# Optimization experiments

Measured on AMD Instinct MI355X. Metric: run time of the kernel, lower is better.

## Reference

```python
import jax, jax.numpy as jnp
import numpy as np

N_USERS, N_BOOKS, D, E, B = 50000, 100000, 128, 500000, 16384
N = N_USERS + N_BOOKS
EPS = 1e-5


def _gcn_conv(x, W, b, src, dst, n):
    # PyG GCNConv: linear transform, then symmetric-normalized aggregation with self-loops.
    h = x @ W  # [N, D]
    ones = jnp.ones(src.shape[0], h.dtype)
    deg = jax.ops.segment_sum(ones, dst, num_segments=n) + 1.0  # +1 for self-loop
    dis = jax.lax.rsqrt(deg)  # deg^{-1/2}
    norm = dis[src] * dis[dst]  # [E]
    agg = jax.ops.segment_sum(h[src] * norm[:, None], dst, num_segments=n)
    agg = agg + h * (dis * dis)[:, None]  # self-loop contribution, norm = deg_i^{-1}
    return agg + b


def _batch_norm(x, gamma, beta):
    m = x.mean(axis=0)
    v = x.var(axis=0)  # biased, as in torch BN normalization
    return (x - m) * jax.lax.rsqrt(v + EPS) * gamma + beta


def setup_inputs() -> dict:
    key = jax.random.key(0)
    ks = jax.random.split(key, 12)
    edge_index = jax.random.randint(ks[0], (2, E), 0, N)
    x = jax.random.normal(ks[1], (1, 1), dtype=jnp.float32)  # unused by forward
    src_nodes = jax.random.randint(ks[2], (B,), 0, N_USERS)
    dst_nodes = jax.random.randint(ks[3], (B,), N_USERS, N)
    user_emb = 0.01 * jax.random.normal(ks[4], (N_USERS, D), dtype=jnp.float32)
    book_emb = 0.01 * jax.random.normal(ks[5], (N_BOOKS, D), dtype=jnp.float32)
    s = 1.0 / np.sqrt(D)
    W1 = jax.random.uniform(ks[6], (D, D), jnp.float32, -s, s)
    b1 = jnp.zeros((D,), jnp.float32)
    W2 = jax.random.uniform(ks[7], (D, D), jnp.float32, -s, s)
    b2 = jnp.zeros((D,), jnp.float32)
    g1 = jnp.ones((D,), jnp.float32)
    be1 = jnp.zeros((D,), jnp.float32)
    g2 = jnp.ones((D,), jnp.float32)
    be2 = jnp.zeros((D,), jnp.float32)
    return {"edge_index": edge_index, "x": x, "src_nodes": src_nodes,
            "dst_nodes": dst_nodes, "user_emb": user_emb, "book_emb": book_emb,
            "W1": W1, "b1": b1, "g1": g1, "be1": be1,
            "W2": W2, "b2": b2, "g2": g2, "be2": be2}


def reference(edge_index, x, src_nodes, dst_nodes, user_emb, book_emb,
              W1, b1, g1, be1, W2, b2, g2, be2):
    esrc, edst = edge_index[0], edge_index[1]
    h = jnp.concatenate([user_emb, book_emb], axis=0)  # [N, D]
    h = _gcn_conv(h, W1, b1, esrc, edst, N)
    h = jax.nn.relu(_batch_norm(h, g1, be1))
    h = _gcn_conv(h, W2, b2, esrc, edst, N)
    h = jax.nn.relu(_batch_norm(h, g2, be2))
    ratings = jnp.sum(h[src_nodes] * h[dst_nodes], axis=1)  # [B]
    return ratings
```

## Files before the change

### kernel.cpp

```cpp
#include <hip/hip_runtime.h>
#include <hip/hip_bf16.h>

#define NN      150000
#define NUSERS  50000
#define DD      128
#define EE      500000
#define BB      16384
#define NSLICE  32
#define ESTRIDE 32

using short8  = __attribute__((ext_vector_type(8))) short;
using ushort8 = __attribute__((ext_vector_type(8))) unsigned short;
using f32x4   = __attribute__((ext_vector_type(4))) float;

typedef __attribute__((address_space(1))) const unsigned int glb_u32;
typedef __attribute__((address_space(3))) unsigned int       lds_u32;

__device__ __forceinline__ short f2bf(float v) {
    __hip_bfloat16 b = __float2bfloat16(v);
    return __builtin_bit_cast(short, b);
}
__device__ __forceinline__ float bf2f(unsigned short b) {
    return __uint_as_float(((unsigned)b) << 16);
}

__global__ __launch_bounds__(256) void prep_k(int4* __restrict__ zbase, int zn4, int zb,
                                              const float* __restrict__ W1,
                                              const float* __restrict__ W2,
                                              short* __restrict__ F1,
                                              short* __restrict__ F2) {
    int b = blockIdx.x;
    if (b < zb) {
        int i = b * 256 + threadIdx.x;
        if (i < zn4) zbase[i] = make_int4(0, 0, 0, 0);
        return;
    }
    int idx = (b - zb) * 256 + threadIdx.x;
    int m = idx >> 14;
    int i = idx & 16383;
    int e  = i & 7;
    int l  = (i >> 3) & 63;
    int kk = (i >> 9) & 3;
    int ct = i >> 11;
    int k = kk * 32 + (l >> 4) * 8 + e;
    int c = ct * 16 + (l & 15);
    const float* W = m ? W2 : W1;
    short*       F = m ? F2 : F1;
    F[i] = f2bf(W[k * DD + c]);
}

__global__ __launch_bounds__(256) void countfill_k(const int* __restrict__ src,
                                                   const int* __restrict__ dst,
                                                   int* __restrict__ cnt,
                                                   int* __restrict__ sedge,
                                                   const int* __restrict__ srcn,
                                                   const int* __restrict__ dstn,
                                                   unsigned char* __restrict__ flags) {
    int e = blockIdx.x * 256 + threadIdx.x;
    if (e < EE) {
        int d = dst[e], s = src[e];
        int pos = atomicAdd(&cnt[d], 1);
        if (pos > ESTRIDE - 1) pos = ESTRIDE - 1;
        sedge[(size_t)d * ESTRIDE + pos] = s;
    }
    if (e < BB) { flags[srcn[e]] = 1; flags[dstn[e]] = 1; }
}

__global__ __launch_bounds__(256) void dis_k(const int* __restrict__ cnt,
                                             float* __restrict__ dis) {
    int i = blockIdx.x * 256 + threadIdx.x;
    if (i < NN) dis[i] = rsqrtf((float)cnt[i] + 1.0f);
}

template<int MODE>
__global__ __launch_bounds__(128) void gemm_mfma_k(const float* __restrict__ A0,
                                                   const float* __restrict__ A1,
                                                   int nsplit,
                                                   const unsigned short* __restrict__ Ab,
                                                   const float* __restrict__ coefs,
                                                   const short* __restrict__ Wfrag,
                                                   unsigned short* __restrict__ hout) {
    constexpr int ROWB  = (MODE == 0) ? 528 : 272;
    constexpr int PAY   = (MODE == 0) ? 512 : 256;
    constexpr int TILEB = 32 * ROWB;
    constexpr int NCH   = TILEB / 16;
    constexpr int FULLR = NCH / 128;

    __shared__ __align__(16) char smem[TILEB];

    int t    = threadIdx.x;
    int wave = t >> 6;
    int lane = t & 63;
    int kgrp = lane >> 4;
    int lrow = lane & 15;
    int r0   = blockIdx.x * 32;

#pragma unroll
    for (int r = 0; r < FULLR; ++r) {
        int chunk = r * 128 + t;
        int o     = chunk * 16;
        int row   = o / ROWB;
        int inner = o - row * ROWB;
        if (inner >= PAY) inner = 0;
        int gr = r0 + row; if (gr > NN - 1) gr = NN - 1;
        const char* src;
        if (MODE == 0) src = (const char*)((gr < nsplit) ? (A0 + (size_t)gr * DD)
                                                         : (A1 + (size_t)(gr - nsplit) * DD)) + inner;
        else           src = (const char*)(Ab + (size_t)gr * DD) + inner;
        lds_u32* dst = (lds_u32*)(smem + (r * 128 + wave * 64) * 16);
        __builtin_amdgcn_global_load_lds((glb_u32*)src, dst, 16, 0, 0);
    }
    if (wave == 0 && lane < 32) {
        int chunk = FULLR * 128 + lane;
        int o     = chunk * 16;
        int row   = o / ROWB;
        int inner = o - row * ROWB;
        if (inner >= PAY) inner = 0;
        int gr = r0 + row; if (gr > NN - 1) gr = NN - 1;
        const char* src;
        if (MODE == 0) src = (const char*)((gr < nsplit) ? (A0 + (size_t)gr * DD)
                                                         : (A1 + (size_t)(gr - nsplit) * DD)) + inner;
        else           src = (const char*)(Ab + (size_t)gr * DD) + inner;
        lds_u32* dst = (lds_u32*)(smem + FULLR * 128 * 16);
        __builtin_amdgcn_global_load_lds((glb_u32*)src, dst, 16, 0, 0);
    }
    __syncthreads();

    const char* arow = smem + (wave * 16 + lrow) * ROWB;

    f32x4 acc[8];
#pragma unroll
    for (int ct = 0; ct < 8; ++ct) acc[ct] = (f32x4){0.f, 0.f, 0.f, 0.f};

    const short8* wf = (const short8*)Wfrag;

#pragma unroll
    for (int kk = 0; kk < 4; ++kk) {
        short8 rfrag;
        if (MODE == 0) {
            f32x4 va = *(const f32x4*)(arow + kk * 128 + kgrp * 32);
            f32x4 vb = *(const f32x4*)(arow + kk * 128 + kgrp * 32 + 16);
#pragma unroll
            for (int j = 0; j < 4; ++j) { rfrag[j] = f2bf(va[j]); rfrag[4 + j] = f2bf(vb[j]); }
        } else {
            int d0 = kk * 32 + kgrp * 8;
            ushort8 u = *(const ushort8*)(arow + kk * 64 + kgrp * 16);
            f32x4 s1 = *(const f32x4*)(coefs + d0);
            f32x4 s2 = *(const f32x4*)(coefs + d0 + 4);
            f32x4 t1 = *(const f32x4*)(coefs + 128 + d0);
            f32x4 t2 = *(const f32x4*)(coefs + 128 + d0 + 4);
#pragma unroll
            for (int j = 0; j < 4; ++j) {
                rfrag[j]     = f2bf(fmaxf(bf2f(u[j])     * s1[j] + t1[j], 0.f));
                rfrag[4 + j] = f2bf(fmaxf(bf2f(u[4 + j]) * s2[j] + t2[j], 0.f));
            }
        }
#pragma unroll
        for (int ct = 0; ct < 8; ++ct) {
            short8 wfr = wf[(ct * 4 + kk) * 64 + lane];
            acc[ct] = __builtin_amdgcn_mfma_f32_16x16x32_bf16(wfr, rfrag, acc[ct], 0, 0, 0);
        }
    }

    int row = r0 + wave * 16 + lrow;
    if (row < NN) {
        size_t rb = (size_t)row * DD;
#pragma unroll
        for (int ct = 0; ct < 8; ++ct) {
            int col = ct * 16 + kgrp * 4;
            unsigned p0 = (unsigned)(unsigned short)f2bf(acc[ct][0])
                        | ((unsigned)(unsigned short)f2bf(acc[ct][1]) << 16);
            unsigned p1 = (unsigned)(unsigned short)f2bf(acc[ct][2])
                        | ((unsigned)(unsigned short)f2bf(acc[ct][3]) << 16);
            uint2 p; p.x = p0; p.y = p1;
            *(uint2*)(hout + rb + col) = p;
        }
    }
}

template<int PRUNE>
__global__ __launch_bounds__(256) void gather_k(const unsigned short* __restrict__ h,
                                                const int* __restrict__ sedge,
                                                const int* __restrict__ cnt,
                                                const float* __restrict__ dis,
                                                const unsigned char* __restrict__ flags,
                                                unsigned short* __restrict__ aggb,
                                                float* __restrict__ sums) {
    int t = threadIdx.x;
    int l = t & 15;
    int rg = t >> 4;
    int row = blockIdx.x * 16 + rg;
    int len = min(cnt[row], ESTRIDE);
    const int* se = sedge + (size_t)row * ESTRIDE;
    const ushort8* hp = (const ushort8*)h;

    float acc[8];
#pragma unroll
    for (int j = 0; j < 8; ++j) acc[j] = 0.f;

    for (int base = 0; base < len; base += 4) {
        int i1 = min(base + 1, len - 1);
        int i2 = min(base + 2, len - 1);
        int i3 = min(base + 3, len - 1);
        int s0 = se[base], s1 = se[i1], s2 = se[i2], s3 = se[i3];
        ushort8 h0 = hp[(size_t)s0 * 16 + l];
        ushort8 h1 = hp[(size_t)s1 * 16 + l];
        ushort8 h2 = hp[(size_t)s2 * 16 + l];
        ushort8 h3 = hp[(size_t)s3 * 16 + l];
        float w0 = dis[s0];
        float w1 = (base + 1 < len) ? dis[s1] : 0.f;
        float w2 = (base + 2 < len) ? dis[s2] : 0.f;
        float w3 = (base + 3 < len) ? dis[s3] : 0.f;
#pragma unroll
        for (int j = 0; j < 8; ++j) {
            acc[j] += w0 * bf2f(h0[j]) + w1 * bf2f(h1[j])
                    + w2 * bf2f(h2[j]) + w3 * bf2f(h3[j]);
        }
    }
    float d  = dis[row];
    float d2 = d * d;
    ushort8 hs = hp[(size_t)row * 16 + l];
    float r[8];
    ushort8 o;
#pragma unroll
    for (int j = 0; j < 8; ++j) {
        r[j] = d * acc[j] + d2 * bf2f(hs[j]);
        o[j] = (unsigned short)f2bf(r[j]);
    }
    if (!PRUNE || flags[row])
        ((ushort8*)aggb)[(size_t)row * 16 + l] = o;

    __shared__ float red[16][132];
    float* slice = sums + (blockIdx.x & (NSLICE - 1)) * 256;
    int co = l * 8;
#pragma unroll
    for (int j = 0; j < 8; ++j) red[rg][co + j] = r[j];
    __syncthreads();
    if (t < 128) {
        float a = 0.f;
#pragma unroll
        for (int g = 0; g < 16; ++g) a += red[g][t];
        atomicAdd(&slice[t], a);
    }
    __syncthreads();
#pragma unroll
    for (int j = 0; j < 8; ++j) red[rg][co + j] = r[j] * r[j];
    __syncthreads();
    if (t < 128) {
        float a = 0.f;
#pragma unroll
        for (int g = 0; g < 16; ++g) a += red[g][t];
        atomicAdd(&slice[128 + t], a);
    }
}

__global__ void bncoef_k(const float* __restrict__ sums,
                         const float* __restrict__ gamma,
                         const float* __restrict__ beta,
                         float* __restrict__ coefs) {
    int c = threadIdx.x;
    if (c >= DD) return;
    float s = 0.f, s2 = 0.f;
#pragma unroll
    for (int g = 0; g < NSLICE; ++g) {
        s  += sums[g * 256 + c];
        s2 += sums[g * 256 + 128 + c];
    }
    const float n = (float)NN;
    float m  = s / n;
    float v  = s2 / n - m * m;
    float is = rsqrtf(v + 1e-5f);
    float sc = gamma[c] * is;
    coefs[c] = sc;
    coefs[128 + c] = beta[c] - m * sc;
}

__global__ __launch_bounds__(256) void ratings_k(const unsigned short* __restrict__ x,
                                                 const int* __restrict__ srcn,
                                                 const int* __restrict__ dstn,
                                                 const float* __restrict__ coefs,
                                                 float* __restrict__ out) {
    int wid  = (blockIdx.x * 256 + threadIdx.x) >> 6;
    int lane = threadIdx.x & 63;
    if (wid >= BB) return;
    int u = srcn[wid], v = dstn[wid];
    const ushort2* xp = (const ushort2*)x;
    ushort2 a = xp[(size_t)u * 64 + lane];
    ushort2 b = xp[(size_t)v * 64 + lane];
    float2 sc = ((const float2*)coefs)[lane];
    float2 sh = ((const float2*)(coefs + 128))[lane];
    float ax = fmaxf(bf2f(a.x) * sc.x + sh.x, 0.f);
    float ay = fmaxf(bf2f(a.y) * sc.y + sh.y, 0.f);
    float bx = fmaxf(bf2f(b.x) * sc.x + sh.x, 0.f);
    float by = fmaxf(bf2f(b.y) * sc.y + sh.y, 0.f);
    float acc = ax * bx + ay * by;
#pragma unroll
    for (int off = 32; off; off >>= 1) acc += __shfl_down(acc, off, 64);
    if (lane == 0) out[wid] = acc;
}

extern "C" void kernel_launch(void* const* d_in, const int* in_sizes, int n_in,
                              void* d_out, int out_size, void* d_ws, size_t ws_size,
                              hipStream_t stream) {
    const int*   edge  = (const int*)d_in[0];
    const int*   esrc  = edge;
    const int*   edst  = edge + EE;
    const int*   srcn  = (const int*)d_in[2];
    const int*   dstn  = (const int*)d_in[3];
    const float* uemb  = (const float*)d_in[4];
    const float* bemb  = (const float*)d_in[5];
    const float* W1    = (const float*)d_in[6];
    const float* g1    = (const float*)d_in[8];
    const float* be1   = (const float*)d_in[9];
    const float* W2    = (const float*)d_in[10];
    const float* g2    = (const float*)d_in[12];
    const float* be2   = (const float*)d_in[13];
    float* out = (float*)d_out;

    unsigned short* aggb   = (unsigned short*)d_ws;
    unsigned short* hbuf   = aggb + (size_t)NN * DD;
    int*            cnt    = (int*)(hbuf + (size_t)NN * DD);
    unsigned char*  flags  = (unsigned char*)(cnt + 150016);
    float*          sums1  = (float*)(flags + 150016);
    float*          sums2  = sums1 + NSLICE * 256;
    float*          dis    = sums2 + NSLICE * 256;
    int*            sedge  = (int*)(dis + 150016);
    short*          Wf1    = (short*)(sedge + (size_t)150016 * ESTRIDE);
    short*          Wf2    = Wf1 + 16384;
    float*          coef1  = (float*)(Wf2 + 16384);
    float*          coef2  = coef1 + 256;

    const int zn4   = (150016 * 4 + 150016 + 2 * NSLICE * 256 * 4) / 16;
    const int zb    = (zn4 + 255) / 256;
    const int egrid = (EE + 255) / 256;
    const int ngrid = (NN + 255) / 256;
    const int ggrid = (NN + 31) / 32;
    const int agrid = NN / 16;

    prep_k<<<zb + 128, 256, 0, stream>>>((int4*)cnt, zn4, zb, W1, W2, Wf1, Wf2);
    countfill_k<<<egrid, 256, 0, stream>>>(esrc, edst, cnt, sedge, srcn, dstn, flags);
    dis_k<<<ngrid, 256, 0, stream>>>(cnt, dis);

    gemm_mfma_k<0><<<ggrid, 128, 0, stream>>>(uemb, bemb, NUSERS, nullptr, nullptr, Wf1, hbuf);
    gather_k<0><<<agrid, 256, 0, stream>>>(hbuf, sedge, cnt, dis, flags, aggb, sums1);
    bncoef_k<<<1, 128, 0, stream>>>(sums1, g1, be1, coef1);

    gemm_mfma_k<1><<<ggrid, 128, 0, stream>>>(nullptr, nullptr, 0, aggb, coef1, Wf2, hbuf);
    gather_k<1><<<agrid, 256, 0, stream>>>(hbuf, sedge, cnt, dis, flags, aggb, sums2);
    bncoef_k<<<1, 128, 0, stream>>>(sums2, g2, be2, coef2);

    ratings_k<<<BB / 4, 256, 0, stream>>>(aggb, srcn, dstn, coef2, out);
}
```

Baseline: 168.7 us.

## Stage weight fragments in LDS and read activation rows directly from global

The GEMM kernel now stages the 32 KB pre-swizzled weight fragments into LDS with async global-to-LDS loads, instead of staging the activation tile there. Each lane loads its A row straight from global memory into registers. Blocks grow from 128 to 256 threads covering 64 rows, which halves the grid. The goal is to stop re-reading the W fragments from global/L2 in every block. The cost is that each block now loads 32 KB of W into LDS, and the A reads per lane are strided and less coalesced.

After: 159.4 us. 1.06x faster.

```diff
diff --git a/kernel.cpp b/kernel.cpp
--- a/kernel.cpp
+++ b/kernel.cpp
@@ -73,78 +73,55 @@
 }
 
 template<int MODE>
-__global__ __launch_bounds__(128) void gemm_mfma_k(const float* __restrict__ A0,
+__global__ __launch_bounds__(256) void gemm_mfma_k(const float* __restrict__ A0,
                                                    const float* __restrict__ A1,
                                                    int nsplit,
                                                    const unsigned short* __restrict__ Ab,
                                                    const float* __restrict__ coefs,
                                                    const short* __restrict__ Wfrag,
                                                    unsigned short* __restrict__ hout) {
-    constexpr int ROWB  = (MODE == 0) ? 528 : 272;
-    constexpr int PAY   = (MODE == 0) ? 512 : 256;
-    constexpr int TILEB = 32 * ROWB;
-    constexpr int NCH   = TILEB / 16;
-    constexpr int FULLR = NCH / 128;
-
-    __shared__ __align__(16) char smem[TILEB];
+    __shared__ __align__(16) char smem[32768];
 
     int t    = threadIdx.x;
     int wave = t >> 6;
     int lane = t & 63;
     int kgrp = lane >> 4;
     int lrow = lane & 15;
-    int r0   = blockIdx.x * 32;
-
-#pragma unroll
-    for (int r = 0; r < FULLR; ++r) {
-        int chunk = r * 128 + t;
-        int o     = chunk * 16;
-        int row   = o / ROWB;
-        int inner = o - row * ROWB;
-        if (inner >= PAY) inner = 0;
-        int gr = r0 + row; if (gr > NN - 1) gr = NN - 1;
-        const char* src;
-        if (MODE == 0) src = (const char*)((gr < nsplit) ? (A0 + (size_t)gr * DD)
-                                                         : (A1 + (size_t)(gr - nsplit) * DD)) + inner;
-        else           src = (const char*)(Ab + (size_t)gr * DD) + inner;
-        lds_u32* dst = (lds_u32*)(smem + (r * 128 + wave * 64) * 16);
+
+#pragma unroll
+    for (int r = 0; r < 8; ++r) {
+        const char* src = (const char*)Wfrag + (r * 256 + t) * 16;
+        lds_u32* dst = (lds_u32*)(smem + (r * 256 + wave * 64) * 16);
         __builtin_amdgcn_global_load_lds((glb_u32*)src, dst, 16, 0, 0);
     }
-    if (wave == 0 && lane < 32) {
-        int chunk = FULLR * 128 + lane;
-        int o     = chunk * 16;
-        int row   = o / ROWB;
-        int inner = o - row * ROWB;
-        if (inner >= PAY) inner = 0;
-        int gr = r0 + row; if (gr > NN - 1) gr = NN - 1;
-        const char* src;
-        if (MODE == 0) src = (const char*)((gr < nsplit) ? (A0 + (size_t)gr * DD)
-                                                         : (A1 + (size_t)(gr - nsplit) * DD)) + inner;
-        else           src = (const char*)(Ab + (size_t)gr * DD) + inner;
-        lds_u32* dst = (lds_u32*)(smem + FULLR * 128 * 16);
-        __builtin_amdgcn_global_load_lds((glb_u32*)src, dst, 16, 0, 0);
-    }
+
+    int row = blockIdx.x * 64 + wave * 16 + lrow;
+    int lr = row > NN - 1 ? NN - 1 : row;
+    const float* arow = nullptr;
+    const unsigned short* brow = nullptr;
+    if (MODE == 0) arow = (lr < nsplit) ? A0 + (size_t)lr * DD
+                                        : A1 + (size_t)(lr - nsplit) * DD;
+    else           brow = Ab + (size_t)lr * DD;
+
+    f32x4 acc[8];
+#pragma unroll
+    for (int ct = 0; ct < 8; ++ct) acc[ct] = (f32x4){0.f, 0.f, 0.f, 0.f};
+
     __syncthreads();
 
-    const char* arow = smem + (wave * 16 + lrow) * ROWB;
-
-    f32x4 acc[8];
-#pragma unroll
-    for (int ct = 0; ct < 8; ++ct) acc[ct] = (f32x4){0.f, 0.f, 0.f, 0.f};
-
-    const short8* wf = (const short8*)Wfrag;
+    const short8* wf = (const short8*)smem;
 
 #pragma unroll
     for (int kk = 0; kk < 4; ++kk) {
+        int d0 = kk * 32 + kgrp * 8;
         short8 rfrag;
         if (MODE == 0) {
-            f32x4 va = *(const f32x4*)(arow + kk * 128 + kgrp * 32);
-            f32x4 vb = *(const f32x4*)(arow + kk * 128 + kgrp * 32 + 16);
+            f32x4 va = *(const f32x4*)(arow + d0);
+            f32x4 vb = *(const f32x4*)(arow + d0 + 4);
 #pragma unroll
             for (int j = 0; j < 4; ++j) { rfrag[j] = f2bf(va[j]); rfrag[4 + j] = f2bf(vb[j]); }
         } else {
-            int d0 = kk * 32 + kgrp * 8;
-            ushort8 u = *(const ushort8*)(arow + kk * 64 + kgrp * 16);
+            ushort8 u = *(const ushort8*)(brow + d0);
             f32x4 s1 = *(const f32x4*)(coefs + d0);
             f32x4 s2 = *(const f32x4*)(coefs + d0 + 4);
             f32x4 t1 = *(const f32x4*)(coefs + 128 + d0);
@@ -162,7 +139,6 @@
         }
     }
 
-    int row = r0 + wave * 16 + lrow;
     if (row < NN) {
         size_t rb = (size_t)row * DD;
 #pragma unroll
@@ -334,18 +310,18 @@
     const int zb    = (zn4 + 255) / 256;
     const int egrid = (EE + 255) / 256;
     const int ngrid = (NN + 255) / 256;
-    const int ggrid = (NN + 31) / 32;
+    const int ggrid = (NN + 63) / 64;
     const int agrid = NN / 16;
 
     prep_k<<<zb + 128, 256, 0, stream>>>((int4*)cnt, zn4, zb, W1, W2, Wf1, Wf2);
     countfill_k<<<egrid, 256, 0, stream>>>(esrc, edst, cnt, sedge, srcn, dstn, flags);
     dis_k<<<ngrid, 256, 0, stream>>>(cnt, dis);
 
-    gemm_mfma_k<0><<<ggrid, 128, 0, stream>>>(uemb, bemb, NUSERS, nullptr, nullptr, Wf1, hbuf);
+    gemm_mfma_k<0><<<ggrid, 256, 0, stream>>>(uemb, bemb, NUSERS, nullptr, nullptr, Wf1, hbuf);
     gather_k<0><<<agrid, 256, 0, stream>>>(hbuf, sedge, cnt, dis, flags, aggb, sums1);
     bncoef_k<<<1, 128, 0, stream>>>(sums1, g1, be1, coef1);
 
-    gemm_mfma_k<1><<<ggrid, 128, 0, stream>>>(nullptr, nullptr, 0, aggb, coef1, Wf2, hbuf);
+    gemm_mfma_k<1><<<ggrid, 256, 0, stream>>>(nullptr, nullptr, 0, aggb, coef1, Wf2, hbuf);
     gather_k<1><<<agrid, 256, 0, stream>>>(hbuf, sedge, cnt, dis, flags, aggb, sums2);
     bncoef_k<<<1, 128, 0, stream>>>(sums2, g2, be2, coef2);
 
```
